# Performance work log

Measured on AMD Instinct MI355X. Metric: run time of the kernel, lower is better.

The kernel has to match this reference:

```python
import jax, jax.numpy as jnp
import numpy as np

BLOCK = 8
WIN = 3
PAD = WIN - 1


def _dct_mat(b, dtype):
    # Orthonormal DCT-II matrix: D[k, n] = s_k * sqrt(2/b) * cos(pi*(2n+1)k/(2b))
    n = np.arange(b)
    k = n[:, None]
    D = np.sqrt(2.0 / b) * np.cos(np.pi * (2 * n[None, :] + 1) * k / (2 * b))
    D[0, :] *= 1.0 / np.sqrt(2.0)
    return jnp.asarray(D, dtype=dtype)


def setup_inputs() -> dict:
    key = jax.random.key(0)
    k1, k2 = jax.random.split(key)
    x = jax.random.normal(k1, (8, 64, 256, 256), dtype=jnp.float32)
    conv_w = jax.random.normal(k2, (64, 64, WIN), dtype=jnp.float32) * 0.05
    conv_b = jnp.zeros((64,), dtype=jnp.float32)
    return {"x": x, "conv_w": conv_w, "conv_b": conv_b}


def reference(x, conv_w, conv_b):
    b = BLOCK
    bsz, ch, H, W = x.shape
    nH, nW = H // b, W // b
    n = nH * nW
    D = _dct_mat(b, x.dtype)

    # blockify: (bsz, ch, n_blocks, b, b)
    blk = x.reshape(bsz, ch, nH, b, nW, b).transpose(0, 1, 2, 4, 3, 5)
    blk = blk.reshape(bsz, ch, n, b, b)

    # block 2D DCT: D @ X @ D^T
    coef = jnp.einsum('kn,bcxnm,lm->bcxkl', D, blk, D)
    coef = coef.reshape(bsz, ch, n, b * b)

    # FreqConv: causal-right-padded Conv1d over the b*b frequency axis
    y = coef.transpose(0, 2, 1, 3).reshape(bsz * n, ch, b * b)
    y = jnp.pad(y, ((0, 0), (0, 0), (0, PAD)))
    y = jax.lax.conv_general_dilated(
        y, conv_w, window_strides=(1,), padding=[(0, 0)],
        dimension_numbers=('NCH', 'OIH', 'NCH'), feature_group_count=1)
    y = y + conv_b[None, :, None]
    out_ch = y.shape[1]
    y = y.reshape(bsz, n, out_ch, b * b).transpose(0, 2, 1, 3)

    # block 2D IDCT: D^T @ X @ D
    y = y.reshape(bsz, out_ch, n, b, b)
    img = jnp.einsum('kn,bcxkl,lm->bcxnm', D, y, D)

    # deblockify back to (bsz, out_ch, H, W)
    img = img.reshape(bsz, out_ch, nH, nW, b, b).transpose(0, 1, 2, 4, 3, 5)
    return img.reshape(bsz, out_ch, H, W)
```

## Files before the change

### kernel.cpp

```cpp
#include <hip/hip_runtime.h>


#define THREADS 256
#define HW 256
#define CH 64
#define CT_ROW 72
#define CT_SAMPLE (66 * CT_ROW)
#define XB_SH 8192
#define LDS_BYTES ((XB_SH + 4 * CT_SAMPLE) * 2)

typedef __attribute__((ext_vector_type(8))) short short8b;
typedef __attribute__((ext_vector_type(4))) float f32x4;
typedef __attribute__((ext_vector_type(4))) unsigned short us4;

__device__ inline unsigned short f2bf(float f) {
    unsigned u = __builtin_bit_cast(unsigned, f);
    u += 0x7FFFu + ((u >> 16) & 1u);
    return (unsigned short)(u >> 16);
}

__device__ __constant__ static const float D8[8][8] = {
  { 0.3535533906f, 0.3535533906f, 0.3535533906f, 0.3535533906f, 0.3535533906f, 0.3535533906f, 0.3535533906f, 0.3535533906f },
  { 0.4903926402f, 0.4157348062f, 0.2777851165f, 0.0975451610f,-0.0975451610f,-0.2777851165f,-0.4157348062f,-0.4903926402f },
  { 0.4619397663f, 0.1913417162f,-0.1913417162f,-0.4619397663f,-0.4619397663f,-0.1913417162f, 0.1913417162f, 0.4619397663f },
  { 0.4157348062f,-0.0975451610f,-0.4903926402f,-0.2777851165f, 0.2777851165f, 0.4903926402f, 0.0975451610f,-0.4157348062f },
  { 0.3535533906f,-0.3535533906f,-0.3535533906f, 0.3535533906f, 0.3535533906f,-0.3535533906f,-0.3535533906f, 0.3535533906f },
  { 0.2777851165f,-0.4903926402f, 0.0975451610f, 0.4157348062f,-0.4157348062f,-0.0975451610f, 0.4903926402f,-0.2777851165f },
  { 0.1913417162f,-0.4619397663f, 0.4619397663f,-0.1913417162f,-0.1913417162f, 0.4619397663f,-0.4619397663f, 0.1913417162f },
  { 0.0975451610f,-0.2777851165f, 0.4157348062f,-0.4903926402f, 0.4903926402f,-0.4157348062f, 0.2777851165f,-0.0975451610f },
};

__global__ __launch_bounds__(256)
void prep_kernel(const float* __restrict__ conv_w, unsigned short* __restrict__ ws16) {
    int idx = blockIdx.x * 256 + threadIdx.x;
    int j = idx & 7, lane = (idx >> 3) & 63;
    int lrr = lane & 15, lqq = lane >> 4;
    if (idx < 4096) {
        int nk = idx >> 9, n = nk >> 1, kc = nk & 1;
        int t = n * 16 + lrr, s = kc * 32 + lqq * 8 + j;
        ws16[idx] = f2bf(D8[t >> 3][s >> 3] * D8[t & 7][s & 7]);
    } else if (idx < 8192) {
        int i2 = idx - 4096;
        int mk = i2 >> 9, m = mk >> 1, kc = mk & 1;
        int s = m * 16 + lrr, t = kc * 32 + lqq * 8 + j;
        ws16[idx] = f2bf(D8[t >> 3][s >> 3] * D8[t & 7][s & 7]);
    } else if (idx < 20480) {
        int i3 = idx - 8192;
        int grp = i3 >> 9, m = grp & 3, hc = (grp >> 2) & 1, w = grp >> 3;
        int o = m * 16 + lrr, i = hc * 32 + lqq * 8 + j;
        ws16[idx] = f2bf(conv_w[o * 192 + i * 3 + w]);
    }
}

__global__ __launch_bounds__(THREADS, 3)
void dct_freq_conv_kernel(const float* __restrict__ x,
                          const unsigned short* __restrict__ ws16,
                          const float* __restrict__ conv_b,
                          float* __restrict__ out)
{
    extern __shared__ char smem[];
    unsigned short* Xb = (unsigned short*)smem;
    float*          Ou = (float*)smem;
    unsigned short* Ct = (unsigned short*)smem + XB_SH;
    const unsigned short* Tf = ws16;
    const unsigned short* Uf = ws16 + 4096;
    const unsigned short* Wf = ws16 + 8192;

    const int tid = threadIdx.x;
    const int wid = tid >> 6, lane = tid & 63;
    const int lr = lane & 15, lq = lane >> 4;
    const int bz = blockIdx.z, by = blockIdx.y, bx = blockIdx.x;
    unsigned short* CtP = Ct + wid * CT_SAMPLE;

    if (lane < 36) *(us4*)&CtP[64 * CT_ROW + lane * 4] = (us4){0, 0, 0, 0};

    float bias[4];
    #pragma unroll
    for (int m = 0; m < 4; ++m) bias[m] = conv_b[m * 16 + lr];

    auto stage = [&](int h) {
        #pragma unroll
        for (int rep = 0; rep < 8; ++rep) {
            int f4 = rep * 256 + tid;
            int cl = f4 & 7, rl = (f4 >> 3) & 3, c = f4 >> 5;
            const float* gp = x + ((size_t)(bz * 64 + c) * 256 + by * 8 + h * 4 + rl) * 256
                                + bx * 32 + cl * 4;
            float4 v = *(const float4*)gp;
            us4 pk; pk[0] = f2bf(v.x); pk[1] = f2bf(v.y); pk[2] = f2bf(v.z); pk[3] = f2bf(v.w);
            int smp = cl >> 1, kk = rl * 8 + (cl & 1) * 4;
            *(us4*)&Xb[smp * 2048 + c * 32 + (kk ^ ((c & 3) << 3))] = pk;
        }
    };

    f32x4 acc[4][4];
    #pragma unroll
    for (int m = 0; m < 4; ++m)
        #pragma unroll
        for (int n = 0; n < 4; ++n) acc[m][n] = (f32x4){0.f, 0.f, 0.f, 0.f};

    auto gemm1_step = [&](int kc) {
        short8b a[4], b[4];
        #pragma unroll
        for (int m = 0; m < 4; ++m) {
            const int cA = m * 16 + lr;
            a[m] = *(const short8b*)&Xb[wid * 2048 + cA * 32 + ((lq * 8) ^ ((cA & 3) << 3))];
        }
        #pragma unroll
        for (int n = 0; n < 4; ++n)
            b[n] = *(const short8b*)&Tf[((n * 2 + kc) * 64 + lane) * 8];
        #pragma unroll
        for (int m = 0; m < 4; ++m)
            #pragma unroll
            for (int n = 0; n < 4; ++n)
                acc[m][n] = __builtin_amdgcn_mfma_f32_16x16x32_bf16(a[m], b[n], acc[m][n], 0, 0, 0);
    };

    stage(0);
    __syncthreads();
    gemm1_step(0);
    __syncthreads();
    stage(1);
    __syncthreads();
    gemm1_step(1);

    #pragma unroll
    for (int m = 0; m < 4; ++m)
        #pragma unroll
        for (int n = 0; n < 4; ++n) {
            us4 pk;
            #pragma unroll
            for (int j = 0; j < 4; ++j) pk[j] = f2bf(acc[m][n][j]);
            *(us4*)&CtP[(n * 16 + lr) * CT_ROW + m * 16 + lq * 4] = pk;
        }

    f32x4 acc2[4][4];
    #pragma unroll
    for (int n = 0; n < 4; ++n)
        #pragma unroll
        for (int m = 0; m < 4; ++m) acc2[n][m] = (f32x4){0.f, 0.f, 0.f, 0.f};

    #pragma unroll
    for (int kc = 0; kc < 6; ++kc) {
        const int w  = kc >> 1;
        const int i0 = (kc & 1) * 32 + lq * 8;
        short8b a[4], b[4];
        #pragma unroll
        for (int n = 0; n < 4; ++n)
            a[n] = *(const short8b*)&CtP[(n * 16 + lr + w) * CT_ROW + i0];
        #pragma unroll
        for (int m = 0; m < 4; ++m)
            b[m] = *(const short8b*)&Wf[((kc * 4 + m) * 64 + lane) * 8];
        #pragma unroll
        for (int n = 0; n < 4; ++n)
            #pragma unroll
            for (int m = 0; m < 4; ++m)
                acc2[n][m] = __builtin_amdgcn_mfma_f32_16x16x32_bf16(a[n], b[m], acc2[n][m], 0, 0, 0);
    }
    #pragma unroll
    for (int n = 0; n < 4; ++n)
        #pragma unroll
        for (int m = 0; m < 4; ++m) {
            us4 pk;
            #pragma unroll
            for (int j = 0; j < 4; ++j) pk[j] = f2bf(acc2[n][m][j] + bias[m]);
            *(us4*)&CtP[(m * 16 + lr) * CT_ROW + n * 16 + lq * 4] = pk;
        }

    #pragma unroll
    for (int mg = 0; mg < 2; ++mg) {
        f32x4 a3[2][4];
        #pragma unroll
        for (int mh = 0; mh < 2; ++mh)
            #pragma unroll
            for (int ct = 0; ct < 4; ++ct) a3[mh][ct] = (f32x4){0.f, 0.f, 0.f, 0.f};

        #pragma unroll
        for (int kc = 0; kc < 2; ++kc) {
            short8b ua[2], yb[4];
            #pragma unroll
            for (int mh = 0; mh < 2; ++mh)
                ua[mh] = *(const short8b*)&Uf[(((mg * 2 + mh) * 2 + kc) * 64 + lane) * 8];
            #pragma unroll
            for (int ct = 0; ct < 4; ++ct)
                yb[ct] = *(const short8b*)&CtP[(ct * 16 + lr) * CT_ROW + kc * 32 + lq * 8];
            #pragma unroll
            for (int mh = 0; mh < 2; ++mh)
                #pragma unroll
                for (int ct = 0; ct < 4; ++ct)
                    a3[mh][ct] = __builtin_amdgcn_mfma_f32_16x16x32_bf16(ua[mh], yb[ct], a3[mh][ct], 0, 0, 0);
        }

        #pragma unroll
        for (int mh = 0; mh < 2; ++mh) {
            const int q = mg * 2 + mh;
            #pragma unroll
            for (int ct = 0; ct < 4; ++ct)
                *(f32x4*)&Ou[wid * 1024 + (ct * 16 + lr) * 16 + ((lq ^ wid) & 3) * 4] = a3[mh][ct];
            __syncthreads();
            #pragma unroll
            for (int rep = 0; rep < 4; ++rep) {
                int gl = tid & 1, smp = (tid >> 1) & 3, c = (rep & 1) * 32 + (tid >> 3);
                int gh = rep >> 1, g = gh * 2 + gl;
                f32x4 v = *(const f32x4*)&Ou[smp * 1024 + c * 16 + ((g ^ smp) & 3) * 4];
                int r = q * 2 + gh;
                *(float4*)(out + ((size_t)(bz * 64 + c) * 256 + by * 8 + r) * 256
                           + bx * 32 + smp * 8 + gl * 4)
                    = make_float4(v[0], v[1], v[2], v[3]);
            }
            __syncthreads();
        }
    }
}

extern "C" void kernel_launch(void* const* d_in, const int* in_sizes, int n_in,
                              void* d_out, int out_size, void* d_ws, size_t ws_size,
                              hipStream_t stream) {
    const float* x  = (const float*)d_in[0];
    const float* cw = (const float*)d_in[1];
    const float* cb = (const float*)d_in[2];
    float* o        = (float*)d_out;
    unsigned short* ws16 = (unsigned short*)d_ws;

    prep_kernel<<<dim3(80), dim3(256), 0, stream>>>(cw, ws16);

    hipFuncSetAttribute(reinterpret_cast<const void*>(dct_freq_conv_kernel),
                        hipFuncAttributeMaxDynamicSharedMemorySize,
                        (int)LDS_BYTES);
    dim3 grid(8, 32, 8);
    dct_freq_conv_kernel<<<grid, dim3(THREADS), LDS_BYTES, stream>>>(x, ws16, cb, o);
}
```

Before: 258.4 us.

## Prefetch second input half into registers, swizzle LDS layouts, batch output epilogue

Global loads for the second half of the input tile are now issued into registers before the first GEMM step runs, so that memory latency overlaps MFMA work. All LDS buffers switch to byte-addressed XOR-swizzled layouts with 128-byte rows instead of padded rows, aiming to avoid bank conflicts on both reads and writes. The inverse-DCT stage now computes all four output groups at once and writes them out in two batches with coalesced full-row stores, which cuts the number of block barriers. The cost is higher register pressure from the prefetch buffer and the larger accumulator set, which could lower occupancy under the 3-blocks launch bound.

After: 251.6 us. -2.6%, faster.

```diff
diff --git a/kernel.cpp b/kernel.cpp
--- a/kernel.cpp
+++ b/kernel.cpp
@@ -2,12 +2,9 @@
 
 
 #define THREADS 256
-#define HW 256
-#define CH 64
-#define CT_ROW 72
-#define CT_SAMPLE (66 * CT_ROW)
-#define XB_SH 8192
-#define LDS_BYTES ((XB_SH + 4 * CT_SAMPLE) * 2)
+#define XB_BYTES 16384
+#define CT_STRIDE_B 8448
+#define LDS_BYTES (XB_BYTES + 4 * CT_STRIDE_B)
 
 typedef __attribute__((ext_vector_type(8))) short short8b;
 typedef __attribute__((ext_vector_type(4))) float f32x4;
@@ -36,8 +33,8 @@
     int j = idx & 7, lane = (idx >> 3) & 63;
     int lrr = lane & 15, lqq = lane >> 4;
     if (idx < 4096) {
-        int nk = idx >> 9, n = nk >> 1, kc = nk & 1;
-        int t = n * 16 + lrr, s = kc * 32 + lqq * 8 + j;
+        int nk = idx >> 9, n = nk >> 1, h = nk & 1;
+        int t = n * 16 + lrr, s = h * 32 + lqq * 8 + j;
         ws16[idx] = f2bf(D8[t >> 3][s >> 3] * D8[t & 7][s & 7]);
     } else if (idx < 8192) {
         int i2 = idx - 4096;
@@ -59,9 +56,8 @@
                           float* __restrict__ out)
 {
     extern __shared__ char smem[];
-    unsigned short* Xb = (unsigned short*)smem;
-    float*          Ou = (float*)smem;
-    unsigned short* Ct = (unsigned short*)smem + XB_SH;
+    char* XbB = smem;
+    char* CtB = smem + XB_BYTES;
     const unsigned short* Tf = ws16;
     const unsigned short* Uf = ws16 + 4096;
     const unsigned short* Wf = ws16 + 8192;
@@ -70,145 +66,167 @@
     const int wid = tid >> 6, lane = tid & 63;
     const int lr = lane & 15, lq = lane >> 4;
     const int bz = blockIdx.z, by = blockIdx.y, bx = blockIdx.x;
-    unsigned short* CtP = Ct + wid * CT_SAMPLE;
-
-    if (lane < 36) *(us4*)&CtP[64 * CT_ROW + lane * 4] = (us4){0, 0, 0, 0};
+    char* CtP = CtB + wid * CT_STRIDE_B;
+
+    if (lane < 32) {
+        int rp = lane >> 4, cq = lane & 15;
+        int byte = (64 + rp) * 128 + (((cq >> 1) ^ rp) << 4) + (cq & 1) * 8;
+        *(us4*)(CtP + byte) = (us4){0, 0, 0, 0};
+    }
 
     float bias[4];
     #pragma unroll
     for (int m = 0; m < 4; ++m) bias[m] = conv_b[m * 16 + lr];
 
-    auto stage = [&](int h) {
+    auto stage_load = [&](int h, int rep) -> float4 {
+        int f4 = rep * 256 + tid;
+        int cl = f4 & 7, rl = (f4 >> 3) & 3, c = f4 >> 5;
+        return *(const float4*)(x + ((size_t)(bz * 64 + c) * 256 + by * 8 + h * 4 + rl) * 256
+                                + bx * 32 + cl * 4);
+    };
+    auto stage_store = [&](int rep, float4 v) {
+        int f4 = rep * 256 + tid;
+        int cl = f4 & 7, rl = (f4 >> 3) & 3, c = f4 >> 5;
+        int smp = cl >> 1;
+        us4 pk; pk[0] = f2bf(v.x); pk[1] = f2bf(v.y); pk[2] = f2bf(v.z); pk[3] = f2bf(v.w);
+        *(us4*)(XbB + smp * 4096 + c * 64 + ((rl ^ smp ^ ((c >> 1) & 3)) << 4)
+                + (cl & 1) * 8) = pk;
+    };
+
+    f32x4 acc1[4][4];
+    #pragma unroll
+    for (int m = 0; m < 4; ++m)
+        #pragma unroll
+        for (int n = 0; n < 4; ++n) acc1[m][n] = (f32x4){0.f, 0.f, 0.f, 0.f};
+
+    auto gemm1_step = [&](int h) {
+        short8b a[4], b[4];
+        #pragma unroll
+        for (int m = 0; m < 4; ++m) {
+            const int c = m * 16 + lr;
+            a[m] = *(const short8b*)(XbB + wid * 4096 + c * 64
+                                     + ((lq ^ wid ^ ((lr >> 1) & 3)) << 4));
+        }
+        #pragma unroll
+        for (int n = 0; n < 4; ++n)
+            b[n] = *(const short8b*)&Tf[((n * 2 + h) * 64 + lane) * 8];
+        #pragma unroll
+        for (int m = 0; m < 4; ++m)
+            #pragma unroll
+            for (int n = 0; n < 4; ++n)
+                acc1[m][n] = __builtin_amdgcn_mfma_f32_16x16x32_bf16(a[m], b[n], acc1[m][n], 0, 0, 0);
+    };
+
+    #pragma unroll
+    for (int rep = 0; rep < 8; ++rep) stage_store(rep, stage_load(0, rep));
+    __syncthreads();
+    float4 xr[8];
+    #pragma unroll
+    for (int rep = 0; rep < 8; ++rep) xr[rep] = stage_load(1, rep);
+    gemm1_step(0);
+    __syncthreads();
+    #pragma unroll
+    for (int rep = 0; rep < 8; ++rep) stage_store(rep, xr[rep]);
+    __syncthreads();
+    gemm1_step(1);
+
+    #pragma unroll
+    for (int m = 0; m < 4; ++m)
+        #pragma unroll
+        for (int n = 0; n < 4; ++n) {
+            int row = n * 16 + lr;
+            int byte = row * 128 + (((m * 2 + (lq >> 1)) ^ (lr & 7)) << 4) + (lq & 1) * 8;
+            us4 pk;
+            #pragma unroll
+            for (int j = 0; j < 4; ++j) pk[j] = f2bf(acc1[m][n][j]);
+            *(us4*)(CtP + byte) = pk;
+        }
+
+    f32x4 acc2[4][4];
+    #pragma unroll
+    for (int n = 0; n < 4; ++n)
+        #pragma unroll
+        for (int m = 0; m < 4; ++m) acc2[n][m] = (f32x4){0.f, 0.f, 0.f, 0.f};
+
+    #pragma unroll
+    for (int kc = 0; kc < 6; ++kc) {
+        const int w = kc >> 1;
+        short8b a[4], b[4];
+        #pragma unroll
+        for (int n = 0; n < 4; ++n) {
+            int row = n * 16 + lr + w;
+            int slot = (kc & 1) * 4 + lq;
+            a[n] = *(const short8b*)(CtP + row * 128 + ((slot ^ (row & 7)) << 4));
+        }
+        #pragma unroll
+        for (int m = 0; m < 4; ++m)
+            b[m] = *(const short8b*)&Wf[((kc * 4 + m) * 64 + lane) * 8];
+        #pragma unroll
+        for (int n = 0; n < 4; ++n)
+            #pragma unroll
+            for (int m = 0; m < 4; ++m)
+                acc2[n][m] = __builtin_amdgcn_mfma_f32_16x16x32_bf16(a[n], b[m], acc2[n][m], 0, 0, 0);
+    }
+    #pragma unroll
+    for (int n = 0; n < 4; ++n)
+        #pragma unroll
+        for (int m = 0; m < 4; ++m) {
+            int byte = (m * 16 + lr) * 128 + (((n * 2 + (lq >> 1)) ^ (lr & 7)) << 4) + (lq & 1) * 8;
+            us4 pk;
+            #pragma unroll
+            for (int j = 0; j < 4; ++j) pk[j] = f2bf(acc2[n][m][j] + bias[m]);
+            *(us4*)(CtP + byte) = pk;
+        }
+
+    f32x4 acc3[4][4];
+    #pragma unroll
+    for (int m4 = 0; m4 < 4; ++m4)
+        #pragma unroll
+        for (int ct = 0; ct < 4; ++ct) acc3[m4][ct] = (f32x4){0.f, 0.f, 0.f, 0.f};
+
+    #pragma unroll
+    for (int kc = 0; kc < 2; ++kc) {
+        short8b ua[4], yb[4];
+        #pragma unroll
+        for (int m4 = 0; m4 < 4; ++m4)
+            ua[m4] = *(const short8b*)&Uf[((m4 * 2 + kc) * 64 + lane) * 8];
+        #pragma unroll
+        for (int ct = 0; ct < 4; ++ct) {
+            int row = ct * 16 + lr;
+            int slot = kc * 4 + lq;
+            yb[ct] = *(const short8b*)(CtP + row * 128 + ((slot ^ (row & 7)) << 4));
+        }
+        #pragma unroll
+        for (int m4 = 0; m4 < 4; ++m4)
+            #pragma unroll
+            for (int ct = 0; ct < 4; ++ct)
+                acc3[m4][ct] = __builtin_amdgcn_mfma_f32_16x16x32_bf16(ua[m4], yb[ct], acc3[m4][ct], 0, 0, 0);
+    }
+
+    __syncthreads();
+    char* OuP = smem + wid * 8192;
+    #pragma unroll
+    for (int hh = 0; hh < 2; ++hh) {
+        #pragma unroll
+        for (int mh = 0; mh < 2; ++mh)
+            #pragma unroll
+            for (int ct = 0; ct < 4; ++ct) {
+                int o = ct * 16 + lr;
+                int slot = mh * 4 + lq;
+                *(f32x4*)(OuP + o * 128 + ((slot ^ (o & 7)) << 4)) = acc3[hh * 2 + mh][ct];
+            }
+        __syncthreads();
         #pragma unroll
         for (int rep = 0; rep < 8; ++rep) {
             int f4 = rep * 256 + tid;
-            int cl = f4 & 7, rl = (f4 >> 3) & 3, c = f4 >> 5;
-            const float* gp = x + ((size_t)(bz * 64 + c) * 256 + by * 8 + h * 4 + rl) * 256
-                                + bx * 32 + cl * 4;
-            float4 v = *(const float4*)gp;
-            us4 pk; pk[0] = f2bf(v.x); pk[1] = f2bf(v.y); pk[2] = f2bf(v.z); pk[3] = f2bf(v.w);
-            int smp = cl >> 1, kk = rl * 8 + (cl & 1) * 4;
-            *(us4*)&Xb[smp * 2048 + c * 32 + (kk ^ ((c & 3) << 3))] = pk;
-        }
-    };
-
-    f32x4 acc[4][4];
-    #pragma unroll
-    for (int m = 0; m < 4; ++m)
-        #pragma unroll
-        for (int n = 0; n < 4; ++n) acc[m][n] = (f32x4){0.f, 0.f, 0.f, 0.f};
-
-    auto gemm1_step = [&](int kc) {
-        short8b a[4], b[4];
-        #pragma unroll
-        for (int m = 0; m < 4; ++m) {
-            const int cA = m * 16 + lr;
-            a[m] = *(const short8b*)&Xb[wid * 2048 + cA * 32 + ((lq * 8) ^ ((cA & 3) << 3))];
-        }
-        #pragma unroll
-        for (int n = 0; n < 4; ++n)
-            b[n] = *(const short8b*)&Tf[((n * 2 + kc) * 64 + lane) * 8];
-        #pragma unroll
-        for (int m = 0; m < 4; ++m)
-            #pragma unroll
-            for (int n = 0; n < 4; ++n)
-                acc[m][n] = __builtin_amdgcn_mfma_f32_16x16x32_bf16(a[m], b[n], acc[m][n], 0, 0, 0);
-    };
-
-    stage(0);
-    __syncthreads();
-    gemm1_step(0);
-    __syncthreads();
-    stage(1);
-    __syncthreads();
-    gemm1_step(1);
-
-    #pragma unroll
-    for (int m = 0; m < 4; ++m)
-        #pragma unroll
-        for (int n = 0; n < 4; ++n) {
-            us4 pk;
-            #pragma unroll
-            for (int j = 0; j < 4; ++j) pk[j] = f2bf(acc[m][n][j]);
-            *(us4*)&CtP[(n * 16 + lr) * CT_ROW + m * 16 + lq * 4] = pk;
-        }
-
-    f32x4 acc2[4][4];
-    #pragma unroll
-    for (int n = 0; n < 4; ++n)
-        #pragma unroll
-        for (int m = 0; m < 4; ++m) acc2[n][m] = (f32x4){0.f, 0.f, 0.f, 0.f};
-
-    #pragma unroll
-    for (int kc = 0; kc < 6; ++kc) {
-        const int w  = kc >> 1;
-        const int i0 = (kc & 1) * 32 + lq * 8;
-        short8b a[4], b[4];
-        #pragma unroll
-        for (int n = 0; n < 4; ++n)
-            a[n] = *(const short8b*)&CtP[(n * 16 + lr + w) * CT_ROW + i0];
-        #pragma unroll
-        for (int m = 0; m < 4; ++m)
-            b[m] = *(const short8b*)&Wf[((kc * 4 + m) * 64 + lane) * 8];
-        #pragma unroll
-        for (int n = 0; n < 4; ++n)
-            #pragma unroll
-            for (int m = 0; m < 4; ++m)
-                acc2[n][m] = __builtin_amdgcn_mfma_f32_16x16x32_bf16(a[n], b[m], acc2[n][m], 0, 0, 0);
-    }
-    #pragma unroll
-    for (int n = 0; n < 4; ++n)
-        #pragma unroll
-        for (int m = 0; m < 4; ++m) {
-            us4 pk;
-            #pragma unroll
-            for (int j = 0; j < 4; ++j) pk[j] = f2bf(acc2[n][m][j] + bias[m]);
-            *(us4*)&CtP[(m * 16 + lr) * CT_ROW + n * 16 + lq * 4] = pk;
-        }
-
-    #pragma unroll
-    for (int mg = 0; mg < 2; ++mg) {
-        f32x4 a3[2][4];
-        #pragma unroll
-        for (int mh = 0; mh < 2; ++mh)
-            #pragma unroll
-            for (int ct = 0; ct < 4; ++ct) a3[mh][ct] = (f32x4){0.f, 0.f, 0.f, 0.f};
-
-        #pragma unroll
-        for (int kc = 0; kc < 2; ++kc) {
-            short8b ua[2], yb[4];
-            #pragma unroll
-            for (int mh = 0; mh < 2; ++mh)
-                ua[mh] = *(const short8b*)&Uf[(((mg * 2 + mh) * 2 + kc) * 64 + lane) * 8];
-            #pragma unroll
-            for (int ct = 0; ct < 4; ++ct)
-                yb[ct] = *(const short8b*)&CtP[(ct * 16 + lr) * CT_ROW + kc * 32 + lq * 8];
-            #pragma unroll
-            for (int mh = 0; mh < 2; ++mh)
-                #pragma unroll
-                for (int ct = 0; ct < 4; ++ct)
-                    a3[mh][ct] = __builtin_amdgcn_mfma_f32_16x16x32_bf16(ua[mh], yb[ct], a3[mh][ct], 0, 0, 0);
-        }
-
-        #pragma unroll
-        for (int mh = 0; mh < 2; ++mh) {
-            const int q = mg * 2 + mh;
-            #pragma unroll
-            for (int ct = 0; ct < 4; ++ct)
-                *(f32x4*)&Ou[wid * 1024 + (ct * 16 + lr) * 16 + ((lq ^ wid) & 3) * 4] = a3[mh][ct];
-            __syncthreads();
-            #pragma unroll
-            for (int rep = 0; rep < 4; ++rep) {
-                int gl = tid & 1, smp = (tid >> 1) & 3, c = (rep & 1) * 32 + (tid >> 3);
-                int gh = rep >> 1, g = gh * 2 + gl;
-                f32x4 v = *(const f32x4*)&Ou[smp * 1024 + c * 16 + ((g ^ smp) & 3) * 4];
-                int r = q * 2 + gh;
-                *(float4*)(out + ((size_t)(bz * 64 + c) * 256 + by * 8 + r) * 256
-                           + bx * 32 + smp * 8 + gl * 4)
-                    = make_float4(v[0], v[1], v[2], v[3]);
-            }
-            __syncthreads();
-        }
+            int gl = f4 & 7, c = (f4 >> 3) & 63, rr = f4 >> 9;
+            int smp = gl >> 1;
+            int slot = rr * 2 + (gl & 1);
+            f32x4 v = *(const f32x4*)(smem + smp * 8192 + c * 128 + ((slot ^ (c & 7)) << 4));
+            *(float4*)(out + ((size_t)(bz * 64 + c) * 256 + by * 8 + hh * 4 + rr) * 256
+                       + bx * 32 + gl * 4) = make_float4(v[0], v[1], v[2], v[3]);
+        }
+        if (hh == 0) __syncthreads();
     }
 }
 
```
